# Optimization experiments

Hardware: AMD Instinct MI355X
Metric: run time of the kernel (lower is better)

Reference implementation:

```python
import jax, jax.numpy as jnp
import numpy as np

D = 2  # NUM_DIM (spatial dimension)


def _mlp(x, params, activate_final=False):
    n = len(params)
    for i, (w, b) in enumerate(params):
        x = x @ w + b
        if i < n - 1 or activate_final:
            x = jnp.tanh(x)
    return x


def _glorot(key, shape):
    fan_in, fan_out = shape[0], shape[-1]
    lim = np.sqrt(6.0 / (fan_in + fan_out)).astype(np.float32)
    return jax.random.uniform(key, shape, jnp.float32, -lim, lim)


def setup_inputs() -> dict:
    key = jax.random.key(0)
    ks = iter(jax.random.split(key, 40))
    B, N, M, K, P, C = 4, 32, 64, 16, 128, 2
    AW, TW, W = 64, 256, 128
    inp = {}
    inp['phase_coords'] = jax.random.normal(next(ks), (B, N, 2 * D), jnp.float32)
    inp['boundary_coords'] = jax.random.normal(next(ks), (B, M, 2 * D), jnp.float32)
    inp['boundary'] = jax.random.uniform(next(ks), (B, M), jnp.float32)
    inp['boundary_weights'] = jax.random.uniform(next(ks), (B, M), jnp.float32)
    inp['position_coords'] = jax.random.normal(next(ks), (B, P, D), jnp.float32)
    inp['sigma'] = jax.random.uniform(next(ks), (B, P, C), jnp.float32)
    inp['velocity_coords'] = jax.random.normal(next(ks), (B, K, D), jnp.float32)
    inp['velocity_weights'] = jax.random.uniform(next(ks), (B, K), jnp.float32)
    inp['scattering_kernel'] = jax.random.uniform(next(ks), (B, N, K), jnp.float32)
    inp['self_scattering_kernel'] = jax.random.uniform(next(ks), (B, K, K), jnp.float32)
    # attention MLP: input 2*D + 2 (coords ++ local frame) -> [64, 64, 1]
    inp['aw0'] = _glorot(next(ks), (2 * D + 2, AW)); inp['ab0'] = jnp.zeros((AW,), jnp.float32)
    inp['aw1'] = _glorot(next(ks), (AW, AW)); inp['ab1'] = jnp.zeros((AW,), jnp.float32)
    inp['aw2'] = _glorot(next(ks), (AW, 1)); inp['ab2'] = jnp.zeros((1,), jnp.float32)
    # transport MLP: input 4*D + C -> [256, 256, 128], activate_final=True
    inp['tw0'] = _glorot(next(ks), (4 * D + C, TW)); inp['tb0'] = jnp.zeros((TW,), jnp.float32)
    inp['tw1'] = _glorot(next(ks), (TW, TW)); inp['tb1'] = jnp.zeros((TW,), jnp.float32)
    inp['tw2'] = _glorot(next(ks), (TW, W)); inp['tb2'] = jnp.zeros((W,), jnp.float32)
    # scattering modules: res_block_depth=2 -> one stacked layer + one final layer
    inp['sw0'] = _glorot(next(ks), (W, W))
    inp['sb0'] = jax.random.uniform(next(ks), (W,), jnp.float32, -0.1, 0.1)
    inp['sw1'] = _glorot(next(ks), (W, W))
    inp['sb1'] = jax.random.uniform(next(ks), (W,), jnp.float32, -0.1, 0.1)
    inp['out_w'] = jax.random.uniform(next(ks), (W,), jnp.float32, -0.1, 0.1)
    return inp


def _forward(phase_coords, boundary_coords, boundary, boundary_weights,
             position_coords, sigma, velocity_coords, velocity_weights,
             scattering_kernel, self_scattering_kernel,
             aw0, ab0, aw1, ab1, aw2, ab2,
             tw0, tb0, tw1, tb1, tw2, tb2,
             sw0, sb0, sw1, sb1, out_w):
    B, N, _ = phase_coords.shape
    M = boundary_coords.shape[1]
    K = velocity_coords.shape[1]
    P = position_coords.shape[1]
    C = sigma.shape[-1]
    K1 = K + 1  # phase velocity v plus the Nv quadrature velocities

    x, v = phase_coords[..., :D], phase_coords[..., D:]          # (B,N,D)
    xp, vp = boundary_coords[..., :D], boundary_coords[..., D:]  # (B,M,D)

    # all velocities at which the transport MLP is evaluated: (B,N,K1,D)
    vall = jnp.concatenate(
        [v[:, :, None, :],
         jnp.broadcast_to(velocity_coords[:, None, :, :], (B, N, K, D))], axis=2)

    # ---- CoefficientNet (geometry-masked MLP attention over coeff positions) ----
    coords = jnp.concatenate(
        [jnp.broadcast_to(x[:, :, None, :], (B, N, K1, D)), vall], axis=-1)  # (B,N,K1,2D)
    ang_g = vall / jnp.sqrt(jnp.sum(vall ** 2, axis=-1, keepdims=True) + 1e-16)
    rel = x[:, :, None, :] - position_coords[:, None, :, :]                 # (B,N,P,D)
    rel_dist = jnp.sqrt(jnp.sum(rel ** 2, axis=-1) + 1e-16)                 # (B,N,P)
    pos_local = jnp.einsum('bnpd,bnkd->bnkp', rel, ang_g)                   # (B,N,K1,P)
    ang_local = pos_local / (rel_dist[:, :, None, :] + 1e-8)
    frames = jnp.stack([ang_local, pos_local], axis=-1)                     # (B,N,K1,P,2)
    qk = jnp.concatenate(
        [jnp.broadcast_to(coords[:, :, :, None, :], (B, N, K1, P, 2 * D)), frames], axis=-1)
    logits = _mlp(qk, [(aw0, ab0), (aw1, ab1), (aw2, ab2)])[..., 0]         # (B,N,K1,P)
    attn_w = jax.nn.softmax(jnp.where(pos_local > 0, logits, -1e30), axis=-1)
    coeff = jnp.exp(-jnp.einsum('bnkp,bpc->bnkc', attn_w, sigma))           # (B,N,K1,C)

    # ---- TransportModule: MLP + exp over (B,N,M,K1) ----
    t_in = jnp.concatenate([
        jnp.broadcast_to(x[:, :, None, None, :], (B, N, M, K1, D)),
        jnp.broadcast_to(vall[:, :, None, :, :], (B, N, M, K1, D)),
        jnp.broadcast_to(xp[:, None, :, None, :], (B, N, M, K1, D)),
        jnp.broadcast_to(vp[:, None, :, None, :], (B, N, M, K1, D)),
        jnp.broadcast_to(coeff[:, :, None, :, :], (B, N, M, K1, C)),
    ], axis=-1)
    g = jnp.exp(_mlp(t_in, [(tw0, tb0), (tw1, tb1), (tw2, tb2)], activate_final=True))
    act_v = g[:, :, :, 0, :]       # (B,N,M,W)  at the phase velocity
    act_vstar = g[:, :, :, 1:, :]  # (B,N,M,K,W) at the quadrature velocities

    rw_v = (1.0 - scattering_kernel) * velocity_weights[:, None, :]        # (B,N,K)
    rw_vs = (1.0 - self_scattering_kernel) * velocity_weights[:, None, :]  # (B,K,K)

    def scat_v(act, sw, sb):
        res = jnp.einsum('bnk,bnmkw->bnmw', rw_v, act)
        return jnp.tanh(jnp.einsum('iw,bnmw->bnmi', sw, res) + sb)

    def scat_vs(act, sw, sb):
        res = jnp.einsum('bij,bnmjw->bnmiw', rw_vs, act)
        return jnp.tanh(jnp.einsum('iw,bnmkw->bnmki', sw, res) + sb)

    # layer_stack block (res_block_depth - 1 = 1 layer, shared params within the layer)
    new_v = act_v + scat_v(act_vstar, sw0, sb0)
    act_vstar = act_vstar + scat_vs(act_vstar, sw0, sb0)
    act_v = new_v
    # final scattering module (fresh params) updating act_v with res_weights_v
    green = act_v + scat_v(act_vstar, sw1, sb1)

    gdot = jnp.einsum('bnmw,w->bnm', green, out_w)
    # quadrature over boundary points
    return jnp.einsum('bnm,bm->bn', gdot, boundary * boundary_weights)


def reference(phase_coords, boundary_coords, boundary, boundary_weights,
              position_coords, sigma, velocity_coords, velocity_weights,
              scattering_kernel, self_scattering_kernel,
              aw0, ab0, aw1, ab1, aw2, ab2,
              tw0, tb0, tw1, tb1, tw2, tb2,
              sw0, sb0, sw1, sb1, out_w):
    return _forward(phase_coords, boundary_coords, boundary, boundary_weights,
                    position_coords, sigma, velocity_coords, velocity_weights,
                    scattering_kernel, self_scattering_kernel,
                    aw0, ab0, aw1, ab1, aw2, ab2,
                    tw0, tb0, tw1, tb1, tw2, tb2,
                    sw0, sb0, sw1, sb1, out_w)
```

## Files before the change

### kernel.cpp

```cpp
#include <hip/hip_runtime.h>
#include <hip/hip_bf16.h>

#define BB 4
#define NN 32
#define MM 64
#define KK 16
#define KK1 17
#define PP 128
#define CC 2

typedef unsigned short ushort_t;
typedef unsigned int uint32;
typedef __attribute__((ext_vector_type(8))) short bhalf8;
typedef __attribute__((ext_vector_type(4))) float floatx4;

__device__ __forceinline__ float fast_tanh(float x) {
    float e = __expf(2.0f * x);
    return 1.0f - 2.0f / (e + 1.0f);
}
__device__ __forceinline__ ushort_t f2b(float f) {
    uint32 u = __float_as_uint(f);
    return (ushort_t)((u + 0x8000u) >> 16);
}
__device__ __forceinline__ float b2f(ushort_t h) {
    return __uint_as_float(((uint32)h) << 16);
}

__device__ __forceinline__ bhalf8 tanh_uw(bhalf8 u, bhalf8 w) {
    bhalf8 h;
    #pragma unroll
    for (int j = 0; j < 8; ++j)
        h[j] = (short)f2b(fast_tanh(b2f((ushort_t)u[j]) + b2f((ushort_t)w[j])));
    return h;
}

__global__ void prep_kernel(const float* __restrict__ tw0, const float* __restrict__ tw1,
                            const float* __restrict__ tw2, const float* __restrict__ sw0,
                            const float* __restrict__ sw1, const float* __restrict__ aw0,
                            const float* __restrict__ aw1, const float* __restrict__ tb0,
                            const float* __restrict__ bcoord,
                            ushort_t* __restrict__ W1t, ushort_t* __restrict__ W2t,
                            ushort_t* __restrict__ S0t, ushort_t* __restrict__ S1t,
                            ushort_t* __restrict__ W0a, ushort_t* __restrict__ W1a,
                            ushort_t* __restrict__ w_ws) {
    int i = blockIdx.x * 256 + threadIdx.x;
    if (i < 65536) {
        int nn = i >> 8, k = i & 255;
        W1t[i] = f2b(tw1[k * 256 + nn]);
    } else if (i < 98304) {
        int j = i - 65536; int nn = j >> 8, k = j & 255;
        W2t[j] = f2b(tw2[k * 128 + nn]);
    } else if (i < 114688) {
        S0t[i - 98304] = f2b(sw0[i - 98304]);
    } else if (i < 131072) {
        S1t[i - 114688] = f2b(sw1[i - 114688]);
    } else if (i < 133120) {
        int j = i - 131072; int nn = j >> 5, k = j & 31;
        W0a[j] = (k < 6) ? f2b(aw0[k * 64 + nn]) : (ushort_t)0;
    } else if (i < 137216) {
        int j = i - 133120; int nn = j >> 6, k = j & 63;
        W1a[j] = f2b(aw1[k * 64 + nn]);
    } else if (i < 202752) {
        int j = i - 137216;
        int m = j >> 8, c = j & 255;
        float v = bcoord[m * 4 + 0] * tw0[4 * 256 + c]
                + bcoord[m * 4 + 1] * tw0[5 * 256 + c]
                + bcoord[m * 4 + 2] * tw0[6 * 256 + c]
                + bcoord[m * 4 + 3] * tw0[7 * 256 + c]
                + tb0[c];
        w_ws[j] = f2b(v);
    }
}

#define AH0S 72

__global__ __launch_bounds__(128, 4) void attn_kernel(
    const float* __restrict__ phase, const float* __restrict__ posc,
    const float* __restrict__ sigma, const float* __restrict__ velc,
    const ushort_t* __restrict__ W0a, const ushort_t* __restrict__ W1a,
    const float* __restrict__ ab0, const float* __restrict__ ab1,
    const float* __restrict__ aw2, const float* __restrict__ ab2,
    const float* __restrict__ tw0, ushort_t* __restrict__ u_ws)
{
    __shared__ __align__(16) ushort_t sAH[128 * AH0S];
    __shared__ float sPL[128];
    __shared__ float sLG[128];
    __shared__ float s_red[8];

    const int tid = threadIdx.x;
    const int wave = tid >> 6;
    const int lane = tid & 63;
    const int lrow = lane & 15;
    const int lkg  = lane >> 4;

    const int blk = blockIdx.x;
    const int b = blk / (NN * KK1);
    const int rem = blk % (NN * KK1);
    const int n = rem / KK1;
    const int k = rem % KK1;

    float x0, x1, va0, va1;
    {
        const int p = tid;
        x0 = phase[(b * NN + n) * 4 + 0];
        x1 = phase[(b * NN + n) * 4 + 1];
        if (k == 0) { va0 = phase[(b * NN + n) * 4 + 2]; va1 = phase[(b * NN + n) * 4 + 3]; }
        else { va0 = velc[(b * KK + (k - 1)) * 2 + 0]; va1 = velc[(b * KK + (k - 1)) * 2 + 1]; }
        const float inv = rsqrtf(va0 * va0 + va1 * va1 + 1e-16f);
        const float ag0 = va0 * inv, ag1 = va1 * inv;
        const float px = posc[(b * PP + p) * 2 + 0];
        const float py = posc[(b * PP + p) * 2 + 1];
        const float r0 = x0 - px, r1 = x1 - py;
        const float rd = sqrtf(r0 * r0 + r1 * r1 + 1e-16f);
        const float pl = r0 * ag0 + r1 * ag1;
        const float al = pl / (rd + 1e-8f);
        sPL[p] = pl;
        bhalf8 f0;
        f0[0] = (short)f2b(x0); f0[1] = (short)f2b(x1);
        f0[2] = (short)f2b(va0); f0[3] = (short)f2b(va1);
        f0[4] = (short)f2b(al); f0[5] = (short)f2b(pl);
        f0[6] = 0; f0[7] = 0;
        bhalf8 z = {0, 0, 0, 0, 0, 0, 0, 0};
        *(bhalf8*)&sAH[p * 32 + 0] = f0;
        *(bhalf8*)&sAH[p * 32 + 8] = z;
        *(bhalf8*)&sAH[p * 32 + 16] = z;
        *(bhalf8*)&sAH[p * 32 + 24] = z;
    }
    __syncthreads();

    {
        float b0v[4];
        #pragma unroll
        for (int j = 0; j < 4; ++j) b0v[j] = ab0[j * 16 + lrow];
        bhalf8 a[4];
        #pragma unroll
        for (int mtl = 0; mtl < 4; ++mtl)
            a[mtl] = *(const bhalf8*)&sAH[(wave * 64 + mtl * 16 + lrow) * 32 + lkg * 8];
        __syncthreads();
        #pragma unroll
        for (int j = 0; j < 4; ++j) {
            bhalf8 bf = *(const bhalf8*)(W0a + (j * 16 + lrow) * 32 + lkg * 8);
            #pragma unroll
            for (int mtl = 0; mtl < 4; ++mtl) {
                floatx4 c = {0.f, 0.f, 0.f, 0.f};
                c = __builtin_amdgcn_mfma_f32_16x16x32_bf16(a[mtl], bf, c, 0, 0, 0);
                #pragma unroll
                for (int q = 0; q < 4; ++q) {
                    int row = wave * 64 + mtl * 16 + lkg * 4 + q;
                    sAH[row * AH0S + j * 16 + lrow] = f2b(fast_tanh(c[q] + b0v[j]));
                }
            }
        }
    }
    __syncthreads();

    {
        float b1v[4], w2v[4];
        #pragma unroll
        for (int j = 0; j < 4; ++j) { b1v[j] = ab1[j * 16 + lrow]; w2v[j] = aw2[j * 16 + lrow]; }
        bhalf8 a0[4], a1[4];
        #pragma unroll
        for (int mtl = 0; mtl < 4; ++mtl) {
            int base = (wave * 64 + mtl * 16 + lrow) * AH0S;
            a0[mtl] = *(const bhalf8*)&sAH[base + lkg * 8];
            a1[mtl] = *(const bhalf8*)&sAH[base + 32 + lkg * 8];
        }
        float s[4][4];
        #pragma unroll
        for (int mtl = 0; mtl < 4; ++mtl)
            #pragma unroll
            for (int q = 0; q < 4; ++q) s[mtl][q] = 0.0f;
        #pragma unroll
        for (int j = 0; j < 4; ++j) {
            bhalf8 bf0 = *(const bhalf8*)(W1a + (j * 16 + lrow) * 64 + lkg * 8);
            bhalf8 bf1 = *(const bhalf8*)(W1a + (j * 16 + lrow) * 64 + 32 + lkg * 8);
            #pragma unroll
            for (int mtl = 0; mtl < 4; ++mtl) {
                floatx4 c = {0.f, 0.f, 0.f, 0.f};
                c = __builtin_amdgcn_mfma_f32_16x16x32_bf16(a0[mtl], bf0, c, 0, 0, 0);
                c = __builtin_amdgcn_mfma_f32_16x16x32_bf16(a1[mtl], bf1, c, 0, 0, 0);
                #pragma unroll
                for (int q = 0; q < 4; ++q)
                    s[mtl][q] += fast_tanh(c[q] + b1v[j]) * w2v[j];
            }
        }
        #pragma unroll
        for (int mask = 1; mask <= 8; mask <<= 1)
            #pragma unroll
            for (int mtl = 0; mtl < 4; ++mtl)
                #pragma unroll
                for (int q = 0; q < 4; ++q)
                    s[mtl][q] += __shfl_xor(s[mtl][q], mask, 64);
        if (lrow == 0) {
            #pragma unroll
            for (int mtl = 0; mtl < 4; ++mtl)
                #pragma unroll
                for (int q = 0; q < 4; ++q)
                    sLG[wave * 64 + mtl * 16 + lkg * 4 + q] = s[mtl][q];
        }
    }
    __syncthreads();

    {
        const int p = tid;
        const float ml = (sPL[p] > 0.0f) ? (sLG[p] + ab2[0]) : -1e30f;
        const int wid = wave;
        float mv = ml;
        for (int o = 32; o > 0; o >>= 1) mv = fmaxf(mv, __shfl_xor(mv, o, 64));
        if (lane == 0) s_red[wid] = mv;
        __syncthreads();
        mv = fmaxf(s_red[0], s_red[1]);

        const float ew = __expf(ml - mv);
        float sv = ew;
        for (int o = 32; o > 0; o >>= 1) sv += __shfl_xor(sv, o, 64);
        if (lane == 0) s_red[2 + wid] = sv;
        __syncthreads();
        sv = s_red[2] + s_red[3];
        const float attn = ew / sv;

        float s0 = attn * sigma[(b * PP + p) * 2 + 0];
        float s1 = attn * sigma[(b * PP + p) * 2 + 1];
        for (int o = 32; o > 0; o >>= 1) { s0 += __shfl_xor(s0, o, 64); s1 += __shfl_xor(s1, o, 64); }
        if (lane == 0) { s_red[4 + wid] = s0; s_red[6 + wid] = s1; }
        __syncthreads();

        const float cc0 = __expf(-(s_red[4] + s_red[5]));
        const float cc1 = __expf(-(s_red[6] + s_red[7]));
        const int ubase = ((b * NN + n) * KK1 + k) * 256;
        for (int cc = tid; cc < 256; cc += 128) {
            float uv = x0 * tw0[cc] + x1 * tw0[256 + cc]
                     + va0 * tw0[512 + cc] + va1 * tw0[768 + cc]
                     + cc0 * tw0[2048 + cc] + cc1 * tw0[2304 + cc];
            u_ws[ubase + cc] = f2b(uv);
        }
    }
}

#define H0S  136
#define H1S  264
#define GTSs 40
#define AS2S 136
#define V2S  40

#define U_H0A  0
#define U_GTS  0
#define U_GV   5128
#define U_NEWV 5384
#define U_A2S  5640
#define U_H1A  6152
#define U_AS2  6152
#define U_A3   6152
#define U_V2T  10776
#define U_AS   15128
#define F_BBW  7960
#define F_RED  7962

__global__ __launch_bounds__(256, 4) void transport_kernel(
    const float* __restrict__ boundary, const float* __restrict__ bweights,
    const float* __restrict__ vweights, const float* __restrict__ scat,
    const float* __restrict__ selfscat,
    const ushort_t* __restrict__ W1t, const ushort_t* __restrict__ W2t,
    const ushort_t* __restrict__ S0t, const ushort_t* __restrict__ S1t,
    const float* __restrict__ tb1, const float* __restrict__ tb2,
    const float* __restrict__ sb0, const float* __restrict__ sb1,
    const float* __restrict__ outw,
    const ushort_t* __restrict__ u_ws, const ushort_t* __restrict__ w_ws,
    float* __restrict__ out)
{
    __shared__ __align__(16) ushort_t smem[16160];
    float* smf = (float*)smem;

    const int tid = threadIdx.x;
    const int wave = tid >> 6;
    const int lane = tid & 63;
    const int lrow = lane & 15;
    const int lkg  = lane >> 4;

    const int blk = blockIdx.x;
    const int b  = blk >> 10;
    const int n  = (blk >> 5) & 31;
    const int mg = blk & 31;
    const int m0 = mg * 2;
    const int bn = b * NN + n;

    if (tid < 2)
        smf[F_BBW + tid] = boundary[b * MM + m0 + tid] * bweights[b * MM + m0 + tid];

    for (int idx = tid; idx < 17 * 32; idx += 256) {
        int i = idx >> 5, c = idx & 31;
        float val = 0.0f;
        if (c < 16) {
            float vw = vweights[b * KK + c];
            val = (i < 16) ? (1.0f - selfscat[(b * KK + i) * KK + c]) * vw
                           : (1.0f - scat[bn * KK + c]) * vw;
        }
        smem[U_AS + idx] = f2b(val);
    }

    floatx4 c1[4][3];
    #pragma unroll
    for (int j = 0; j < 4; ++j)
        #pragma unroll
        for (int mt = 0; mt < 3; ++mt) c1[j][mt] = (floatx4){0.f, 0.f, 0.f, 0.f};

    for (int chunk = 0; chunk < 2; ++chunk) {
        if (chunk) __syncthreads();
        {
            const int r0  = tid >> 4;
            const int oct = tid & 15;
            const int co  = chunk * 128 + oct * 8;
            const bhalf8 u0 = *(const bhalf8*)(u_ws + (bn * KK1 + r0) * 256 + co);
            const bhalf8 w0 = *(const bhalf8*)(w_ws + (b * MM + m0) * 256 + co);
            const int ml1 = (r0 >= 1) ? 1 : 0;
            const int k1  = r0 + 16 - 17 * ml1;
            const bhalf8 u1 = *(const bhalf8*)(u_ws + (bn * KK1 + k1) * 256 + co);
            const bhalf8 w1 = *(const bhalf8*)(w_ws + (b * MM + m0 + ml1) * 256 + co);
            bhalf8 u2, w2;
            if (r0 < 2) {
                u2 = *(const bhalf8*)(u_ws + (bn * KK1 + 15 + r0) * 256 + co);
                w2 = *(const bhalf8*)(w_ws + (b * MM + m0 + 1) * 256 + co);
            }
            *(bhalf8*)&smem[U_H0A + r0 * H0S + oct * 8]        = tanh_uw(u0, w0);
            *(bhalf8*)&smem[U_H0A + (16 + r0) * H0S + oct * 8] = tanh_uw(u1, w1);
            if (r0 < 2)
                *(bhalf8*)&smem[U_H0A + (32 + r0) * H0S + oct * 8] = tanh_uw(u2, w2);
        }
        __syncthreads();
        #pragma unroll
        for (int ksl = 0; ksl < 4; ++ksl) {
            bhalf8 a[3];
            #pragma unroll
            for (int mt = 0; mt < 3; ++mt)
                a[mt] = *(const bhalf8*)&smem[U_H0A + (mt * 16 + lrow) * H0S + ksl * 32 + lkg * 8];
            #pragma unroll
            for (int j = 0; j < 4; ++j) {
                bhalf8 bf = *(const bhalf8*)(W1t + ((4 * wave + j) * 16 + lrow) * 256
                                             + chunk * 128 + ksl * 32 + lkg * 8);
                #pragma unroll
                for (int mt = 0; mt < 3; ++mt)
                    c1[j][mt] = __builtin_amdgcn_mfma_f32_16x16x32_bf16(a[mt], bf, c1[j][mt], 0, 0, 0);
            }
        }
    }
    {
        #pragma unroll
        for (int j = 0; j < 4; ++j) {
            float bb = tb1[(4 * wave + j) * 16 + lrow];
            #pragma unroll
            for (int mt = 0; mt < 3; ++mt)
                #pragma unroll
                for (int q = 0; q < 4; ++q) {
                    int row = mt * 16 + lkg * 4 + q;
                    if (row < 34)
                        smem[U_H1A + row * H1S + (4 * wave + j) * 16 + lrow] =
                            f2b(fast_tanh(c1[j][mt][q] + bb));
                }
        }
    }
    __syncthreads();

    {
        bhalf8 z = {0, 0, 0, 0, 0, 0, 0, 0};
        if (tid < 128)       *(bhalf8*)&smem[U_GTS + tid * GTSs + 32] = z;
        else if (tid == 128) *(bhalf8*)&smem[U_GTS + 5120] = z;
    }
    {
        floatx4 c2[2][3];
        #pragma unroll
        for (int j = 0; j < 2; ++j)
            #pragma unroll
            for (int mt = 0; mt < 3; ++mt) c2[j][mt] = (floatx4){0.f, 0.f, 0.f, 0.f};
        #pragma unroll
        for (int ks = 0; ks < 8; ++ks) {
            bhalf8 a[3];
            #pragma unroll
            for (int mt = 0; mt < 3; ++mt) {
                int rr = mt * 16 + lrow;
                if (rr >= 34) rr = 32;
                a[mt] = *(const bhalf8*)&smem[U_H1A + rr * H1S + ks * 32 + lkg * 8];
            }
            #pragma unroll
            for (int j = 0; j < 2; ++j) {
                bhalf8 bf = *(const bhalf8*)(W2t + ((2 * wave + j) * 16 + lrow) * 256 + ks * 32 + lkg * 8);
                #pragma unroll
                for (int mt = 0; mt < 3; ++mt)
                    c2[j][mt] = __builtin_amdgcn_mfma_f32_16x16x32_bf16(a[mt], bf, c2[j][mt], 0, 0, 0);
            }
        }
        #pragma unroll
        for (int j = 0; j < 2; ++j) {
            float bb = tb2[(2 * wave + j) * 16 + lrow];
            #pragma unroll
            for (int mt = 0; mt < 3; ++mt)
                #pragma unroll
                for (int q = 0; q < 4; ++q) {
                    int row = mt * 16 + lkg * 4 + q;
                    if (row < 34) {
                        int ml = (row >= 17);
                        int k = row - ml * 17;
                        int col = (2 * wave + j) * 16 + lrow;
                        float g = __expf(fast_tanh(c2[j][mt][q] + bb));
                        if (k == 0) smem[U_GV + ml * 128 + col] = f2b(g);
                        else        smem[U_GTS + col * GTSs + ml * 16 + (k - 1)] = f2b(g);
                    }
                }
        }
    }
    __syncthreads();

    for (int idx = tid; idx < 512; idx += 256) {
        int r = idx >> 5, c = idx & 31;
        smem[U_A2S + idx] = ((c >> 4) == r) ? smem[U_AS + 16 * 32 + (c & 15)] : (ushort_t)0;
    }
    {
        bhalf8 a0 = *(const bhalf8*)&smem[U_AS + lrow * 32 + lkg * 8];
        bhalf8 a1 = *(const bhalf8*)&smem[U_AS + (16 + lrow) * 32 + lkg * 8];
        for (int m = 0; m < 2; ++m) {
            #pragma unroll
            for (int j = 0; j < 2; ++j) {
                int nt = 2 * wave + j;
                bhalf8 bf = *(const bhalf8*)&smem[U_GTS + (nt * 16 + lrow) * GTSs + m * 16 + lkg * 8];
                #pragma unroll
                for (int mt = 0; mt < 2; ++mt) {
                    floatx4 c = {0.f, 0.f, 0.f, 0.f};
                    c = __builtin_amdgcn_mfma_f32_16x16x32_bf16(mt ? a1 : a0, bf, c, 0, 0, 0);
                    #pragma unroll
                    for (int q = 0; q < 4; ++q) {
                        int ic = mt * 16 + lkg * 4 + q;
                        if (ic < 17) {
                            int r2 = (ic == 16) ? m * 17 : m * 17 + 1 + ic;
                            smem[U_AS2 + r2 * AS2S + nt * 16 + lrow] = f2b(c[q]);
                        }
                    }
                }
            }
        }
    }
    __syncthreads();

    {
        floatx4 c3[2][3];
        #pragma unroll
        for (int j = 0; j < 2; ++j)
            #pragma unroll
            for (int mt = 0; mt < 3; ++mt) c3[j][mt] = (floatx4){0.f, 0.f, 0.f, 0.f};
        #pragma unroll
        for (int ks = 0; ks < 4; ++ks) {
            bhalf8 a[3];
            #pragma unroll
            for (int mt = 0; mt < 3; ++mt)
                a[mt] = *(const bhalf8*)&smem[U_AS2 + (mt * 16 + lrow) * AS2S + ks * 32 + lkg * 8];
            #pragma unroll
            for (int j = 0; j < 2; ++j) {
                bhalf8 bf = *(const bhalf8*)(S0t + ((2 * wave + j) * 16 + lrow) * 128 + ks * 32 + lkg * 8);
                #pragma unroll
                for (int mt = 0; mt < 3; ++mt)
                    c3[j][mt] = __builtin_amdgcn_mfma_f32_16x16x32_bf16(a[mt], bf, c3[j][mt], 0, 0, 0);
            }
        }
        #pragma unroll
        for (int j = 0; j < 2; ++j) {
            float bb = sb0[(2 * wave + j) * 16 + lrow];
            #pragma unroll
            for (int mt = 0; mt < 3; ++mt)
                #pragma unroll
                for (int q = 0; q < 4; ++q) {
                    int r2 = mt * 16 + lkg * 4 + q;
                    if (r2 < 34) {
                        int m = (r2 >= 17);
                        int i2 = r2 - m * 17;
                        int col = (2 * wave + j) * 16 + lrow;
                        float val = fast_tanh(c3[j][mt][q] + bb);
                        if (i2 == 0) {
                            smem[U_NEWV + m * 128 + col] =
                                f2b(b2f(smem[U_GV + m * 128 + col]) + val);
                        } else {
                            int j2 = i2 - 1;
                            smem[U_V2T + col * V2S + m * 16 + j2] =
                                f2b(b2f(smem[U_GTS + col * GTSs + m * 16 + j2]) + val);
                        }
                    }
                }
        }
    }
    __syncthreads();

    {
        bhalf8 a = *(const bhalf8*)&smem[U_A2S + lrow * 32 + lkg * 8];
        #pragma unroll
        for (int j = 0; j < 2; ++j) {
            int nt = 2 * wave + j;
            bhalf8 bf = *(const bhalf8*)&smem[U_V2T + (nt * 16 + lrow) * V2S + lkg * 8];
            floatx4 c = {0.f, 0.f, 0.f, 0.f};
            c = __builtin_amdgcn_mfma_f32_16x16x32_bf16(a, bf, c, 0, 0, 0);
            #pragma unroll
            for (int q = 0; q < 4; ++q) {
                int r = lkg * 4 + q;
                smem[U_A3 + r * AS2S + nt * 16 + lrow] = f2b(c[q]);
            }
        }
    }
    __syncthreads();

    float acc = 0.0f;
    {
        bhalf8 a[4];
        #pragma unroll
        for (int ks = 0; ks < 4; ++ks)
            a[ks] = *(const bhalf8*)&smem[U_A3 + lrow * AS2S + ks * 32 + lkg * 8];
        #pragma unroll
        for (int j = 0; j < 2; ++j) {
            int nt = 2 * wave + j;
            float s1v = sb1[nt * 16 + lrow];
            float owv = outw[nt * 16 + lrow];
            floatx4 c = {0.f, 0.f, 0.f, 0.f};
            #pragma unroll
            for (int ks = 0; ks < 4; ++ks) {
                bhalf8 bf = *(const bhalf8*)(S1t + (nt * 16 + lrow) * 128 + ks * 32 + lkg * 8);
                c = __builtin_amdgcn_mfma_f32_16x16x32_bf16(a[ks], bf, c, 0, 0, 0);
            }
            #pragma unroll
            for (int q = 0; q < 4; ++q) {
                int r = lkg * 4 + q;
                if (r < 2) {
                    int col = nt * 16 + lrow;
                    float green = b2f(smem[U_NEWV + r * 128 + col]) + fast_tanh(c[q] + s1v);
                    acc += green * owv * smf[F_BBW + r];
                }
            }
        }
    }
    for (int o = 32; o > 0; o >>= 1) acc += __shfl_xor(acc, o, 64);
    if (lane == 0) smf[F_RED + wave] = acc;
    __syncthreads();
    if (tid == 0) {
        float tot = smf[F_RED + 0] + smf[F_RED + 1] + smf[F_RED + 2] + smf[F_RED + 3];
        atomicAdd(&out[bn], tot);
    }
}

extern "C" void kernel_launch(void* const* d_in, const int* in_sizes, int n_in,
                              void* d_out, int out_size, void* d_ws, size_t ws_size,
                              hipStream_t stream) {
    const float* phase    = (const float*)d_in[0];
    const float* bcoord   = (const float*)d_in[1];
    const float* boundary = (const float*)d_in[2];
    const float* bweights = (const float*)d_in[3];
    const float* posc     = (const float*)d_in[4];
    const float* sigma    = (const float*)d_in[5];
    const float* velc     = (const float*)d_in[6];
    const float* vweights = (const float*)d_in[7];
    const float* scat     = (const float*)d_in[8];
    const float* selfscat = (const float*)d_in[9];
    const float* aw0 = (const float*)d_in[10];
    const float* ab0 = (const float*)d_in[11];
    const float* aw1 = (const float*)d_in[12];
    const float* ab1 = (const float*)d_in[13];
    const float* aw2 = (const float*)d_in[14];
    const float* ab2 = (const float*)d_in[15];
    const float* tw0 = (const float*)d_in[16];
    const float* tb0 = (const float*)d_in[17];
    const float* tw1 = (const float*)d_in[18];
    const float* tb1 = (const float*)d_in[19];
    const float* tw2 = (const float*)d_in[20];
    const float* tb2 = (const float*)d_in[21];
    const float* sw0 = (const float*)d_in[22];
    const float* sb0 = (const float*)d_in[23];
    const float* sw1 = (const float*)d_in[24];
    const float* sb1 = (const float*)d_in[25];
    const float* outw = (const float*)d_in[26];

    float* out = (float*)d_out;
    char* ws = (char*)d_ws;
    ushort_t* W1t  = (ushort_t*)(ws + 0);
    ushort_t* W2t  = (ushort_t*)(ws + 131072);
    ushort_t* S0t  = (ushort_t*)(ws + 196608);
    ushort_t* S1t  = (ushort_t*)(ws + 229376);
    ushort_t* W0a  = (ushort_t*)(ws + 262144);
    ushort_t* W1a  = (ushort_t*)(ws + 266240);
    ushort_t* u_ws = (ushort_t*)(ws + 274432);
    ushort_t* w_ws = (ushort_t*)(ws + 1388544);

    hipMemsetAsync(d_out, 0, (size_t)out_size * sizeof(float), stream);

    prep_kernel<<<792, 256, 0, stream>>>(tw0, tw1, tw2, sw0, sw1, aw0, aw1, tb0, bcoord,
                                         W1t, W2t, S0t, S1t, W0a, W1a, w_ws);

    attn_kernel<<<BB * NN * KK1, 128, 0, stream>>>(
        phase, posc, sigma, velc, W0a, W1a, ab0, ab1, aw2, ab2, tw0, u_ws);

    transport_kernel<<<BB * NN * 32, 256, 0, stream>>>(
        boundary, bweights, vweights, scat, selfscat,
        W1t, W2t, S0t, S1t, tb1, tb2, sb0, sb1, outw, u_ws, w_ws, out);
}
```

Measured before the change: 283.5 us.

## Shrink transport LDS footprint, prescale tanh inputs, keep per-boundary values in registers

Tanh now uses exp2 and a hardware reciprocal, with the 2*log2(e) factor folded into the biases and the precomputed u/w workspace values so each evaluation saves a multiply and a divide. The transport kernel's second hidden layer is staged through LDS in two halves of 128 columns each, which halves the H1 buffer. The V2T buffer is removed by updating GTS in place, and the GV/NEWV scalars are kept in registers. Together these cut shared memory per block from about 32KB to about 21KB to allow more resident blocks, at the cost of an extra barrier and a slightly changed rounding path.

```diff
diff --git a/kernel.cpp b/kernel.cpp
--- a/kernel.cpp
+++ b/kernel.cpp
@@ -14,10 +14,15 @@
 typedef __attribute__((ext_vector_type(8))) short bhalf8;
 typedef __attribute__((ext_vector_type(4))) float floatx4;
 
-__device__ __forceinline__ float fast_tanh(float x) {
-    float e = __expf(2.0f * x);
-    return 1.0f - 2.0f / (e + 1.0f);
-}
+#define TK  2.885390082f
+#define L2E 1.44269504f
+
+__device__ __forceinline__ float tanh_pre(float xs) {
+    float e = __builtin_amdgcn_exp2f(xs);
+    return fmaf(-2.0f, __builtin_amdgcn_rcpf(e + 1.0f), 1.0f);
+}
+__device__ __forceinline__ float fast_tanh(float x) { return tanh_pre(x * TK); }
+
 __device__ __forceinline__ ushort_t f2b(float f) {
     uint32 u = __float_as_uint(f);
     return (ushort_t)((u + 0x8000u) >> 16);
@@ -30,7 +35,7 @@
     bhalf8 h;
     #pragma unroll
     for (int j = 0; j < 8; ++j)
-        h[j] = (short)f2b(fast_tanh(b2f((ushort_t)u[j]) + b2f((ushort_t)w[j])));
+        h[j] = (short)f2b(tanh_pre(b2f((ushort_t)u[j]) + b2f((ushort_t)w[j])));
     return h;
 }
 
@@ -68,7 +73,7 @@
                 + bcoord[m * 4 + 2] * tw0[6 * 256 + c]
                 + bcoord[m * 4 + 3] * tw0[7 * 256 + c]
                 + tb0[c];
-        w_ws[j] = f2b(v);
+        w_ws[j] = f2b(v * TK);
     }
 }
 
@@ -131,7 +136,7 @@
     {
         float b0v[4];
         #pragma unroll
-        for (int j = 0; j < 4; ++j) b0v[j] = ab0[j * 16 + lrow];
+        for (int j = 0; j < 4; ++j) b0v[j] = ab0[j * 16 + lrow] * TK;
         bhalf8 a[4];
         #pragma unroll
         for (int mtl = 0; mtl < 4; ++mtl)
@@ -147,7 +152,7 @@
                 #pragma unroll
                 for (int q = 0; q < 4; ++q) {
                     int row = wave * 64 + mtl * 16 + lkg * 4 + q;
-                    sAH[row * AH0S + j * 16 + lrow] = f2b(fast_tanh(c[q] + b0v[j]));
+                    sAH[row * AH0S + j * 16 + lrow] = f2b(tanh_pre(fmaf(c[q], TK, b0v[j])));
                 }
             }
         }
@@ -157,7 +162,7 @@
     {
         float b1v[4], w2v[4];
         #pragma unroll
-        for (int j = 0; j < 4; ++j) { b1v[j] = ab1[j * 16 + lrow]; w2v[j] = aw2[j * 16 + lrow]; }
+        for (int j = 0; j < 4; ++j) { b1v[j] = ab1[j * 16 + lrow] * TK; w2v[j] = aw2[j * 16 + lrow]; }
         bhalf8 a0[4], a1[4];
         #pragma unroll
         for (int mtl = 0; mtl < 4; ++mtl) {
@@ -181,7 +186,7 @@
                 c = __builtin_amdgcn_mfma_f32_16x16x32_bf16(a1[mtl], bf1, c, 0, 0, 0);
                 #pragma unroll
                 for (int q = 0; q < 4; ++q)
-                    s[mtl][q] += fast_tanh(c[q] + b1v[j]) * w2v[j];
+                    s[mtl][q] += tanh_pre(fmaf(c[q], TK, b1v[j])) * w2v[j];
             }
         }
         #pragma unroll
@@ -227,34 +232,33 @@
 
         const float cc0 = __expf(-(s_red[4] + s_red[5]));
         const float cc1 = __expf(-(s_red[6] + s_red[7]));
+        const float x0k = x0 * TK, x1k = x1 * TK;
+        const float va0k = va0 * TK, va1k = va1 * TK;
+        const float cc0k = cc0 * TK, cc1k = cc1 * TK;
         const int ubase = ((b * NN + n) * KK1 + k) * 256;
         for (int cc = tid; cc < 256; cc += 128) {
-            float uv = x0 * tw0[cc] + x1 * tw0[256 + cc]
-                     + va0 * tw0[512 + cc] + va1 * tw0[768 + cc]
-                     + cc0 * tw0[2048 + cc] + cc1 * tw0[2304 + cc];
+            float uv = x0k * tw0[cc] + x1k * tw0[256 + cc]
+                     + va0k * tw0[512 + cc] + va1k * tw0[768 + cc]
+                     + cc0k * tw0[2048 + cc] + cc1k * tw0[2304 + cc];
             u_ws[ubase + cc] = f2b(uv);
         }
     }
 }
 
 #define H0S  136
-#define H1S  264
+#define H1S  136
 #define GTSs 40
 #define AS2S 136
-#define V2S  40
 
 #define U_H0A  0
 #define U_GTS  0
-#define U_GV   5128
-#define U_NEWV 5384
-#define U_A2S  5640
-#define U_H1A  6152
-#define U_AS2  6152
-#define U_A3   6152
-#define U_V2T  10776
-#define U_AS   15128
-#define F_BBW  7960
-#define F_RED  7962
+#define U_A2S  5128
+#define U_H1A  5640
+#define U_AS2  5640
+#define U_A3   5640
+#define U_AS   10264
+#define F_RED  3908
+#define F_BBW  5404
 
 __global__ __launch_bounds__(256, 4) void transport_kernel(
     const float* __restrict__ boundary, const float* __restrict__ bweights,
@@ -268,7 +272,7 @@
     const ushort_t* __restrict__ u_ws, const ushort_t* __restrict__ w_ws,
     float* __restrict__ out)
 {
-    __shared__ __align__(16) ushort_t smem[16160];
+    __shared__ __align__(16) ushort_t smem[10816];
     float* smf = (float*)smem;
 
     const int tid = threadIdx.x;
@@ -343,36 +347,38 @@
             }
         }
     }
-    {
-        #pragma unroll
-        for (int j = 0; j < 4; ++j) {
-            float bb = tb1[(4 * wave + j) * 16 + lrow];
+
+    floatx4 c2[2][3];
+    #pragma unroll
+    for (int j = 0; j < 2; ++j)
+        #pragma unroll
+        for (int mt = 0; mt < 3; ++mt) c2[j][mt] = (floatx4){0.f, 0.f, 0.f, 0.f};
+
+    #pragma unroll
+    for (int h = 0; h < 2; ++h) {
+        if (h) __syncthreads();
+        #pragma unroll
+        for (int jj = 0; jj < 2; ++jj) {
+            const int j = 2 * h + jj;
+            const float bb = tb1[(4 * wave + j) * 16 + lrow] * TK;
             #pragma unroll
             for (int mt = 0; mt < 3; ++mt)
                 #pragma unroll
                 for (int q = 0; q < 4; ++q) {
-                    int row = mt * 16 + lkg * 4 + q;
+                    const int row = mt * 16 + lkg * 4 + q;
                     if (row < 34)
-                        smem[U_H1A + row * H1S + (4 * wave + j) * 16 + lrow] =
-                            f2b(fast_tanh(c1[j][mt][q] + bb));
+                        smem[U_H1A + row * H1S + wave * 32 + jj * 16 + lrow] =
+                            f2b(tanh_pre(fmaf(c1[j][mt][q], TK, bb)));
                 }
         }
-    }
-    __syncthreads();
-
-    {
-        bhalf8 z = {0, 0, 0, 0, 0, 0, 0, 0};
-        if (tid < 128)       *(bhalf8*)&smem[U_GTS + tid * GTSs + 32] = z;
-        else if (tid == 128) *(bhalf8*)&smem[U_GTS + 5120] = z;
-    }
-    {
-        floatx4 c2[2][3];
-        #pragma unroll
-        for (int j = 0; j < 2; ++j)
-            #pragma unroll
-            for (int mt = 0; mt < 3; ++mt) c2[j][mt] = (floatx4){0.f, 0.f, 0.f, 0.f};
-        #pragma unroll
-        for (int ks = 0; ks < 8; ++ks) {
+        __syncthreads();
+        if (h == 0) {
+            bhalf8 z = {0, 0, 0, 0, 0, 0, 0, 0};
+            if (tid < 128)       *(bhalf8*)&smem[U_GTS + tid * GTSs + 32] = z;
+            else if (tid == 128) *(bhalf8*)&smem[U_GTS + 5120] = z;
+        }
+        #pragma unroll
+        for (int ks = 0; ks < 4; ++ks) {
             bhalf8 a[3];
             #pragma unroll
             for (int mt = 0; mt < 3; ++mt) {
@@ -381,16 +387,21 @@
                 a[mt] = *(const bhalf8*)&smem[U_H1A + rr * H1S + ks * 32 + lkg * 8];
             }
             #pragma unroll
-            for (int j = 0; j < 2; ++j) {
-                bhalf8 bf = *(const bhalf8*)(W2t + ((2 * wave + j) * 16 + lrow) * 256 + ks * 32 + lkg * 8);
+            for (int j2 = 0; j2 < 2; ++j2) {
+                bhalf8 bf = *(const bhalf8*)(W2t + ((2 * wave + j2) * 16 + lrow) * 256
+                                             + ks * 64 + h * 32 + lkg * 8);
                 #pragma unroll
                 for (int mt = 0; mt < 3; ++mt)
-                    c2[j][mt] = __builtin_amdgcn_mfma_f32_16x16x32_bf16(a[mt], bf, c2[j][mt], 0, 0, 0);
-            }
-        }
+                    c2[j2][mt] = __builtin_amdgcn_mfma_f32_16x16x32_bf16(a[mt], bf, c2[j2][mt], 0, 0, 0);
+            }
+        }
+    }
+
+    float gv0[2] = {0.f, 0.f}, gv1[2] = {0.f, 0.f};
+    {
         #pragma unroll
         for (int j = 0; j < 2; ++j) {
-            float bb = tb2[(2 * wave + j) * 16 + lrow];
+            const float bb = tb2[(2 * wave + j) * 16 + lrow] * TK;
             #pragma unroll
             for (int mt = 0; mt < 3; ++mt)
                 #pragma unroll
@@ -400,8 +411,9 @@
                         int ml = (row >= 17);
                         int k = row - ml * 17;
                         int col = (2 * wave + j) * 16 + lrow;
-                        float g = __expf(fast_tanh(c2[j][mt][q] + bb));
-                        if (k == 0) smem[U_GV + ml * 128 + col] = f2b(g);
+                        float t = tanh_pre(fmaf(c2[j][mt][q], TK, bb));
+                        float g = __builtin_amdgcn_exp2f(t * L2E);
+                        if (k == 0) { if (ml) gv1[j] = g; else gv0[j] = g; }
                         else        smem[U_GTS + col * GTSs + ml * 16 + (k - 1)] = f2b(g);
                     }
                 }
@@ -415,7 +427,7 @@
     }
     {
         bhalf8 a0 = *(const bhalf8*)&smem[U_AS + lrow * 32 + lkg * 8];
-        bhalf8 a1 = *(const bhalf8*)&smem[U_AS + (16 + lrow) * 32 + lkg * 8];
+        bhalf8 a1 = *(const bhalf8*)&smem[U_AS + 16 * 32 + lkg * 8];
         for (int m = 0; m < 2; ++m) {
             #pragma unroll
             for (int j = 0; j < 2; ++j) {
@@ -439,6 +451,7 @@
     }
     __syncthreads();
 
+    float nv0[2] = {0.f, 0.f}, nv1[2] = {0.f, 0.f};
     {
         floatx4 c3[2][3];
         #pragma unroll
@@ -449,8 +462,11 @@
         for (int ks = 0; ks < 4; ++ks) {
             bhalf8 a[3];
             #pragma unroll
-            for (int mt = 0; mt < 3; ++mt)
-                a[mt] = *(const bhalf8*)&smem[U_AS2 + (mt * 16 + lrow) * AS2S + ks * 32 + lkg * 8];
+            for (int mt = 0; mt < 3; ++mt) {
+                int rr = mt * 16 + lrow;
+                if (rr >= 34) rr = 32;
+                a[mt] = *(const bhalf8*)&smem[U_AS2 + rr * AS2S + ks * 32 + lkg * 8];
+            }
             #pragma unroll
             for (int j = 0; j < 2; ++j) {
                 bhalf8 bf = *(const bhalf8*)(S0t + ((2 * wave + j) * 16 + lrow) * 128 + ks * 32 + lkg * 8);
@@ -461,7 +477,7 @@
         }
         #pragma unroll
         for (int j = 0; j < 2; ++j) {
-            float bb = sb0[(2 * wave + j) * 16 + lrow];
+            const float bb = sb0[(2 * wave + j) * 16 + lrow] * TK;
             #pragma unroll
             for (int mt = 0; mt < 3; ++mt)
                 #pragma unroll
@@ -471,14 +487,12 @@
                         int m = (r2 >= 17);
                         int i2 = r2 - m * 17;
                         int col = (2 * wave + j) * 16 + lrow;
-                        float val = fast_tanh(c3[j][mt][q] + bb);
+                        float val = tanh_pre(fmaf(c3[j][mt][q], TK, bb));
                         if (i2 == 0) {
-                            smem[U_NEWV + m * 128 + col] =
-                                f2b(b2f(smem[U_GV + m * 128 + col]) + val);
+                            if (m) nv1[j] = gv1[j] + val; else nv0[j] = gv0[j] + val;
                         } else {
-                            int j2 = i2 - 1;
-                            smem[U_V2T + col * V2S + m * 16 + j2] =
-                                f2b(b2f(smem[U_GTS + col * GTSs + m * 16 + j2]) + val);
+                            int cell = U_GTS + col * GTSs + m * 16 + (i2 - 1);
+                            smem[cell] = f2b(b2f(smem[cell]) + val);
                         }
                     }
                 }
@@ -491,7 +505,7 @@
         #pragma unroll
         for (int j = 0; j < 2; ++j) {
             int nt = 2 * wave + j;
-            bhalf8 bf = *(const bhalf8*)&smem[U_V2T + (nt * 16 + lrow) * V2S + lkg * 8];
+            bhalf8 bf = *(const bhalf8*)&smem[U_GTS + (nt * 16 + lrow) * GTSs + lkg * 8];
             floatx4 c = {0.f, 0.f, 0.f, 0.f};
             c = __builtin_amdgcn_mfma_f32_16x16x32_bf16(a, bf, c, 0, 0, 0);
             #pragma unroll
@@ -512,7 +526,7 @@
         #pragma unroll
         for (int j = 0; j < 2; ++j) {
             int nt = 2 * wave + j;
-            float s1v = sb1[nt * 16 + lrow];
+            float s1v = sb1[nt * 16 + lrow] * TK;
             float owv = outw[nt * 16 + lrow];
             floatx4 c = {0.f, 0.f, 0.f, 0.f};
             #pragma unroll
@@ -520,13 +534,11 @@
                 bhalf8 bf = *(const bhalf8*)(S1t + (nt * 16 + lrow) * 128 + ks * 32 + lkg * 8);
                 c = __builtin_amdgcn_mfma_f32_16x16x32_bf16(a[ks], bf, c, 0, 0, 0);
             }
-            #pragma unroll
-            for (int q = 0; q < 4; ++q) {
-                int r = lkg * 4 + q;
-                if (r < 2) {
-                    int col = nt * 16 + lrow;
-                    float green = b2f(smem[U_NEWV + r * 128 + col]) + fast_tanh(c[q] + s1v);
-                    acc += green * owv * smf[F_BBW + r];
+            if (lkg == 0) {
+                #pragma unroll
+                for (int q = 0; q < 2; ++q) {
+                    float green = (q ? nv1[j] : nv0[j]) + tanh_pre(fmaf(c[q], TK, s1v));
+                    acc += green * owv * smf[F_BBW + q];
                 }
             }
         }
```

Measured after the change: 269.8 us. 4.8% less time.
